# Optimization experiments

Hardware: AMD Instinct MI355X
Metric: run time of the kernel (lower is better)

## Reference

```python
import jax, jax.numpy as jnp
import numpy as np

NUM_USERS = 100000
NUM_ITEMS = 50000
EMB_DIM = 128
NUM_LAYERS = 3
NUM_EDGES = 2000000
BATCH = 8192
REG = 1e-4


def setup_inputs() -> dict:
    key = jax.random.key(0)
    ks = jax.random.split(key, 8)
    N = NUM_USERS + NUM_ITEMS
    user_emb = jax.random.normal(ks[0], (NUM_USERS, EMB_DIM), dtype=jnp.float32) * 0.01
    item_emb = jax.random.normal(ks[1], (NUM_ITEMS, EMB_DIM), dtype=jnp.float32) * 0.01
    edge_row = jax.random.randint(ks[2], (NUM_EDGES,), 0, N, dtype=jnp.int32)
    edge_col = jax.random.randint(ks[3], (NUM_EDGES,), 0, N, dtype=jnp.int32)
    # symmetric-normalized adjacency values are small positives
    edge_val = jax.random.uniform(ks[4], (NUM_EDGES,), dtype=jnp.float32) * 0.1
    user = jax.random.randint(ks[5], (BATCH,), 0, NUM_USERS, dtype=jnp.int32)
    pos = jax.random.randint(ks[6], (BATCH,), 0, NUM_ITEMS, dtype=jnp.int32)
    neg = jax.random.randint(ks[7], (BATCH,), 0, NUM_ITEMS, dtype=jnp.int32)
    return {"user_emb": user_emb, "item_emb": item_emb,
            "edge_row": edge_row, "edge_col": edge_col, "edge_val": edge_val,
            "user": user, "pos": pos, "neg": neg}


def _lightgcn_embedding(user_emb, item_emb, edge_row, edge_col, edge_val):
    N = user_emb.shape[0] + item_emb.shape[0]
    emb = jnp.concatenate([user_emb, item_emb], axis=0)  # [N, D]
    acc = emb
    for _ in range(NUM_LAYERS):
        # SpMM: out[r] += val * emb[c] for each edge (r, c)
        msg = emb[edge_col] * edge_val[:, None]  # [E, D]
        emb = jax.ops.segment_sum(msg, edge_row, num_segments=N)
        acc = acc + emb
    light = acc / jnp.float32(NUM_LAYERS + 1)  # mean over layer outputs
    return light[:NUM_USERS], light[NUM_USERS:]


def reference(user_emb, item_emb, edge_row, edge_col, edge_val, user, pos, neg):
    u_all, i_all = _lightgcn_embedding(user_emb, item_emb, edge_row, edge_col, edge_val)
    u_lat = u_all[user]          # [B, D]
    pos_lat = i_all[pos]
    neg_lat = i_all[neg]
    pos_score = jnp.sum(u_lat * pos_lat, axis=1)
    neg_score = jnp.sum(u_lat * neg_lat, axis=1)
    # L1 regularization on ego (layer-0) embeddings, scalar broadcast onto batch loss
    reg_loss = REG * (jnp.sum(jnp.abs(user_emb[user]))
                      + jnp.sum(jnp.abs(item_emb[pos]))
                      + jnp.sum(jnp.abs(item_emb[neg])))
    batch_loss = jax.nn.softplus(neg_score - pos_score) + reg_loss
    return batch_loss
```

## Files before the change

### kernel.cpp

```cpp
#include <hip/hip_runtime.h>
#include <hip/hip_bf16.h>

#define EMB_D 128
#define BSH 9
#define MAXBUCK 512
#define CHUNKP 2048

typedef float f32x2 __attribute__((ext_vector_type(2)));

__device__ __forceinline__ float bf16_raw_to_f(unsigned short h) {
    return __uint_as_float(((unsigned int)h) << 16);
}
__device__ __forceinline__ float sane(float v) {
    return (v == v && fabsf(v) < 256.0f) ? v : 0.0f;
}
__device__ __forceinline__ float load_f(const void* p, int isf32, size_t idx) {
    return isf32 ? ((const float*)p)[idx]
                 : bf16_raw_to_f(((const unsigned short*)p)[idx]);
}

__device__ __forceinline__ f32x2 cvt2_fp8(unsigned int w) {
    f32x2 r;
    asm("v_cvt_pk_f32_fp8 %0, %1" : "=v"(r) : "v"(w));
    return r;
}
__device__ __forceinline__ unsigned int enc2_fp8(float a, float b) {
    unsigned int r;
    asm("v_cvt_pk_fp8_f32 %0, %1, %2" : "=v"(r) : "v"(a), "v"(b));
    return r & 0xFFFFu;
}
__device__ __forceinline__ unsigned int fp8x4_enc(float a, float b, float c, float d) {
    return enc2_fp8(a, b) | (enc2_fp8(c, d) << 16);
}
__device__ __forceinline__ float fp8_dec_byte(unsigned int b) {
    return cvt2_fp8(b & 0xFFu).x;
}

__global__ void k_detect(const unsigned short* __restrict__ ue,
                         const unsigned short* __restrict__ ie,
                         const unsigned short* __restrict__ ev,
                         int* __restrict__ flags) {
    int a = blockIdx.x;
    const unsigned short* p = (a == 0) ? ue : (a == 1) ? ie : ev;
    int lane = threadIdx.x;
    int cnt = 0;
    #pragma unroll
    for (int k = 0; k < 16; ++k) {
        float v = bf16_raw_to_f(p[k * 64 + lane]);
        if (!(fabsf(v) < 1.0f)) cnt++;
    }
    #pragma unroll
    for (int off = 32; off > 0; off >>= 1)
        cnt += __shfl_down(cnt, off, 64);
    if (lane == 0) flags[a] = (cnt > 64) ? 1 : 0;
}

__global__ __launch_bounds__(256) void k_build_emb8(
        const void* __restrict__ ue, const void* __restrict__ ie,
        const int* __restrict__ flags,
        unsigned char* __restrict__ T, float* __restrict__ S,
        int NU, int N) {
    int gid = blockIdx.x * blockDim.x + threadIdx.x;
    int row = gid >> 5;
    if (row >= N) return;
    int l = gid & 31;
    const void* src; long r; int f;
    if (row < NU) { src = ue; r = row;      f = flags[0]; }
    else          { src = ie; r = row - NU; f = flags[1]; }
    float v0, v1, v2, v3;
    if (f) {
        float4 t = ((const float4*)src)[r * 32 + l];
        v0 = sane(t.x); v1 = sane(t.y); v2 = sane(t.z); v3 = sane(t.w);
    } else {
        ushort4 t = ((const ushort4*)src)[r * 32 + l];
        v0 = sane(bf16_raw_to_f(t.x)); v1 = sane(bf16_raw_to_f(t.y));
        v2 = sane(bf16_raw_to_f(t.z)); v3 = sane(bf16_raw_to_f(t.w));
    }
    float m = fmaxf(fmaxf(fabsf(v0), fabsf(v1)), fmaxf(fabsf(v2), fabsf(v3)));
    #pragma unroll
    for (int off = 1; off < 32; off <<= 1)
        m = fmaxf(m, __shfl_xor(m, off, 64));
    float enc = (m > 0.0f) ? 448.0f / m : 0.0f;
    ((unsigned int*)T)[(size_t)row * 32 + l] =
        fp8x4_enc(v0 * enc, v1 * enc, v2 * enc, v3 * enc);
    if (l == 0) S[row] = (m > 0.0f) ? m * (1.0f / 448.0f) : 0.0f;
}

__global__ void k_zero_flags(int* __restrict__ f, int words, float* __restrict__ reg) {
    int i = blockIdx.x * blockDim.x + threadIdx.x;
    if (i < words) f[i] = 0;
    if (i == 0) reg[0] = 0.0f;
}

__global__ void k_mark_batch(const int* __restrict__ user, const int* __restrict__ pos,
                             const int* __restrict__ neg,
                             const void* __restrict__ ue, const void* __restrict__ ie,
                             const int* __restrict__ flags, int NU, int NI,
                             unsigned char* __restrict__ flag3,
                             unsigned char* __restrict__ flag2,
                             float* __restrict__ regp) {
    __shared__ float sred[2];
    int b = blockIdx.x;
    int d = threadIdx.x;
    int ui = min(max(user[b], 0), NU - 1);
    int pi = min(max(pos[b],  0), NI - 1);
    int ni = min(max(neg[b],  0), NI - 1);
    if (d == 0) {
        flag3[ui] = 1; flag3[NU + pi] = 1; flag3[NU + ni] = 1;
        flag2[ui] = 1; flag2[NU + pi] = 1; flag2[NU + ni] = 1;
    }
    int f0 = flags[0], f1 = flags[1];
    float u = sane(load_f(ue, f0, (size_t)ui * EMB_D + d));
    float p = sane(load_f(ie, f1, (size_t)pi * EMB_D + d));
    float n = sane(load_f(ie, f1, (size_t)ni * EMB_D + d));
    float s = fabsf(u) + fabsf(p) + fabsf(n);
    #pragma unroll
    for (int off = 32; off > 0; off >>= 1)
        s += __shfl_down(s, off, 64);
    if ((d & 63) == 0) sred[d >> 6] = s;
    __syncthreads();
    if (d == 0) regp[b] = sred[0] + sred[1];
}

__global__ void k_reduce_reg(const float* __restrict__ regp, float* __restrict__ reg, int B) {
    __shared__ float ss[256];
    int t = threadIdx.x;
    float s = 0.0f;
    for (int i = t; i < B; i += 256) s += regp[i];
    ss[t] = s;
    __syncthreads();
    for (int off = 128; off > 0; off >>= 1) {
        if (t < off) ss[t] += ss[t + off];
        __syncthreads();
    }
    if (t == 0) reg[0] = ss[0];
}


__global__ __launch_bounds__(256) void k_part_count(
        const int* __restrict__ erow, const int* __restrict__ ecol,
        const unsigned char* __restrict__ flag3, unsigned char* __restrict__ flag2,
        int* __restrict__ bcnt, int E, int N, int nbuck, int NB) {
    __shared__ int lh[MAXBUCK];
    int b = blockIdx.x, t = threadIdx.x;
    for (int i = t; i < MAXBUCK; i += 256) lh[i] = 0;
    __syncthreads();
    int beg = b * CHUNKP;
    int cnt = min(CHUNKP, E - beg);
    for (int p = t; p < cnt; p += 256) {
        int e = beg + p;
        int r = min(max(erow[e], 0), N - 1);
        atomicAdd(&lh[r >> BSH], 1);
        if (flag3[r]) {
            int c = min(max(ecol[e], 0), N - 1);
            flag2[c] = 1;
        }
    }
    __syncthreads();
    for (int i = t; i < nbuck; i += 256) bcnt[(long)i * NB + b] = lh[i];
}

__global__ void k_gscan1(const int* __restrict__ a, int* __restrict__ bsums, int L) {
    __shared__ int ss[256];
    int t = threadIdx.x;
    int base = blockIdx.x * 1024 + t * 4;
    int s = 0;
    #pragma unroll
    for (int j = 0; j < 4; ++j) {
        int idx = base + j;
        if (idx < L) s += a[idx];
    }
    ss[t] = s;
    __syncthreads();
    for (int off = 128; off > 0; off >>= 1) {
        if (t < off) ss[t] += ss[t + off];
        __syncthreads();
    }
    if (t == 0) bsums[blockIdx.x] = ss[0];
}

__global__ void k_gscan2(const int* __restrict__ bsums, int* __restrict__ boffs,
                         int nb, int* __restrict__ rowptrN) {
    __shared__ int ss[256];
    int t = threadIdx.x;
    int base = t * 4;
    int c[4];
    int s = 0;
    #pragma unroll
    for (int j = 0; j < 4; ++j) {
        c[j] = (base + j < nb) ? bsums[base + j] : 0;
        s += c[j];
    }
    ss[t] = s;
    __syncthreads();
    for (int off = 1; off < 256; off <<= 1) {
        int v = (t >= off) ? ss[t - off] : 0;
        __syncthreads();
        ss[t] += v;
        __syncthreads();
    }
    int run = ss[t] - s;
    #pragma unroll
    for (int j = 0; j < 4; ++j) {
        if (base + j < nb) boffs[base + j] = run;
        run += c[j];
    }
    if (t == 255) *rowptrN = ss[255];
}

__global__ void k_gscan3(int* __restrict__ a, const int* __restrict__ boffs, int L) {
    __shared__ int ss[256];
    int t = threadIdx.x;
    int base = blockIdx.x * 1024 + t * 4;
    int c[4];
    int s = 0;
    #pragma unroll
    for (int j = 0; j < 4; ++j) {
        int idx = base + j;
        c[j] = (idx < L) ? a[idx] : 0;
        s += c[j];
    }
    ss[t] = s;
    __syncthreads();
    for (int off = 1; off < 256; off <<= 1) {
        int v = (t >= off) ? ss[t - off] : 0;
        __syncthreads();
        ss[t] += v;
        __syncthreads();
    }
    int run = boffs[blockIdx.x] + ss[t] - s;
    #pragma unroll
    for (int j = 0; j < 4; ++j) {
        int idx = base + j;
        if (idx < L) a[idx] = run;
        run += c[j];
    }
}

__global__ __launch_bounds__(256) void k_part_scatter(
        const int* __restrict__ erow, const int* __restrict__ ecol,
        const void* __restrict__ eval, const int* __restrict__ flags,
        const int* __restrict__ boff,
        unsigned int* __restrict__ part_cv, unsigned short* __restrict__ part_r,
        int E, int N, int nbuck, int NB) {
    __shared__ uint2 lrec[CHUNKP];
    __shared__ unsigned short lidx[CHUNKP];
    __shared__ int hist[MAXBUCK];
    __shared__ int bstart[MAXBUCK];
    __shared__ int ss[256];
    int b = blockIdx.x, t = threadIdx.x;
    int beg = b * CHUNKP;
    int cnt = min(CHUNKP, E - beg);
    for (int i = t; i < MAXBUCK; i += 256) hist[i] = 0;
    __syncthreads();
    int f2 = flags[2];
    for (int p = t; p < cnt; p += 256) {
        int e = beg + p;
        int r = min(max(erow[e], 0), N - 1);
        int c = min(max(ecol[e], 0), N - 1);
        float v = sane(load_f(eval, f2, e));
        if (v < 0.0f) v = 0.0f;
        unsigned int u = __float_as_uint(v);
        unsigned int vb = ((u + 0x10000u) >> 17) & 0x3FFFu;
        lrec[p] = make_uint2((unsigned int)r, ((unsigned int)c << 14) | vb);
        atomicAdd(&hist[r >> BSH], 1);
    }
    __syncthreads();
    int c0 = hist[2 * t], c1 = hist[2 * t + 1];
    int s = c0 + c1;
    ss[t] = s;
    __syncthreads();
    for (int off = 1; off < 256; off <<= 1) {
        int v = (t >= off) ? ss[t - off] : 0;
        __syncthreads();
        ss[t] += v;
        __syncthreads();
    }
    int eb = ss[t] - s;
    bstart[2 * t] = eb;
    bstart[2 * t + 1] = eb + c0;
    hist[2 * t] = eb;
    hist[2 * t + 1] = eb + c0;
    __syncthreads();
    for (int p = t; p < cnt; p += 256) {
        int bin = (int)(lrec[p].x >> BSH);
        int pos = atomicAdd(&hist[bin], 1);
        lidx[pos] = (unsigned short)p;
    }
    __syncthreads();
    for (int i = t; i < nbuck; i += 256)
        hist[i] = boff[(long)i * NB + b] - bstart[i];
    __syncthreads();
    for (int p = t; p < cnt; p += 256) {
        uint2 rec = lrec[lidx[p]];
        int bin = (int)(rec.x >> BSH);
        int o = hist[bin] + p;
        part_cv[o] = rec.y;
        part_r[o] = (unsigned short)(rec.x & 511u);
    }
}

__global__ __launch_bounds__(256) void k_build_csr(
        const unsigned int* __restrict__ part_cv,
        const unsigned short* __restrict__ part_r,
        const int* __restrict__ boff,
        int* __restrict__ row_ptr, unsigned int* __restrict__ sedge,
        int E, int N, int NB, int nbuck) {
    __shared__ int rcnt[256];
    __shared__ int rcur[256];
    __shared__ int ss[256];
    __shared__ int slow;
    int blk = blockIdx.x, t = threadIdx.x;
    int bin = blk >> 1, half = blk & 1;
    int base = boff[(long)bin * NB];
    int next = (bin + 1 < nbuck) ? boff[(long)(bin + 1) * NB] : E;
    int cnt = next - base;
    int r0 = bin << BSH;
    int rlo = half << 8;
    int nrows = min(256, max(0, min(512, N - r0) - rlo));
    rcnt[t] = 0;
    if (t == 0) slow = 0;
    __syncthreads();
    int lowc = 0;
    for (int i = t; i < cnt; i += 256) {
        int pr = part_r[base + i];
        int lp = pr - rlo;
        if (lp >= 0 && lp < 256) atomicAdd(&rcnt[lp], 1);
        else if (pr < rlo) lowc++;
    }
    #pragma unroll
    for (int off = 32; off > 0; off >>= 1)
        lowc += __shfl_down(lowc, off, 64);
    if ((t & 63) == 0 && lowc) atomicAdd(&slow, lowc);
    __syncthreads();
    int c = rcnt[t];
    ss[t] = c;
    __syncthreads();
    for (int off = 1; off < 256; off <<= 1) {
        int v = (t >= off) ? ss[t - off] : 0;
        __syncthreads();
        ss[t] += v;
        __syncthreads();
    }
    int st = ss[t] - c + slow;
    rcur[t] = st;
    __syncthreads();
    if (t < nrows) row_ptr[r0 + rlo + t] = base + st;
    for (int i = t; i < cnt; i += 256) {
        int pr = part_r[base + i];
        int lp = pr - rlo;
        if (lp >= 0 && lp < 256) {
            int pos = atomicAdd(&rcur[lp], 1);
            sedge[base + pos] = part_cv[base + i];
        }
    }
}

__global__ __launch_bounds__(256, 8) void k_spmm_csr8(
        const unsigned char* __restrict__ T, const float* __restrict__ S,
        unsigned char* __restrict__ Td, float* __restrict__ Sd,
        const int* __restrict__ row_ptr, const unsigned int* __restrict__ sedge,
        int N, const unsigned char* __restrict__ skipf, int use_skip) {
    int row = blockIdx.x * (blockDim.x >> 6) + (threadIdx.x >> 6);
    if (row >= N) return;
    if (use_skip && skipf[row] == 0) return;
    int lane = threadIdx.x & 63;
    int beg = row_ptr[row], end = row_ptr[row + 1];
    const unsigned short* Tw = (const unsigned short*)T;
    float a0 = 0.0f, a1 = 0.0f;
    int e = beg;
    for (; e + 3 < end; e += 4) {
        unsigned int s0 = sedge[e],     s1 = sedge[e + 1];
        unsigned int s2 = sedge[e + 2], s3 = sedge[e + 3];
        unsigned int c0 = s0 >> 14, c1 = s1 >> 14, c2 = s2 >> 14, c3 = s3 >> 14;
        unsigned int h0 = Tw[(size_t)c0 * 64 + lane];
        unsigned int h1 = Tw[(size_t)c1 * 64 + lane];
        unsigned int h2 = Tw[(size_t)c2 * 64 + lane];
        unsigned int h3 = Tw[(size_t)c3 * 64 + lane];
        float v0 = __uint_as_float((s0 & 0x3FFFu) << 17) * S[c0];
        float v1 = __uint_as_float((s1 & 0x3FFFu) << 17) * S[c1];
        float v2 = __uint_as_float((s2 & 0x3FFFu) << 17) * S[c2];
        float v3 = __uint_as_float((s3 & 0x3FFFu) << 17) * S[c3];
        f32x2 d;
        d = cvt2_fp8(h0); a0 += v0 * d.x; a1 += v0 * d.y;
        d = cvt2_fp8(h1); a0 += v1 * d.x; a1 += v1 * d.y;
        d = cvt2_fp8(h2); a0 += v2 * d.x; a1 += v2 * d.y;
        d = cvt2_fp8(h3); a0 += v3 * d.x; a1 += v3 * d.y;
    }
    for (; e < end; ++e) {
        unsigned int s0 = sedge[e];
        unsigned int c0 = s0 >> 14;
        unsigned int h0 = Tw[(size_t)c0 * 64 + lane];
        float v0 = __uint_as_float((s0 & 0x3FFFu) << 17) * S[c0];
        f32x2 d = cvt2_fp8(h0);
        a0 += v0 * d.x; a1 += v0 * d.y;
    }
    float m = fmaxf(fabsf(a0), fabsf(a1));
    #pragma unroll
    for (int off = 1; off < 64; off <<= 1)
        m = fmaxf(m, __shfl_xor(m, off, 64));
    float enc = (m > 0.0f) ? 448.0f / m : 0.0f;
    unsigned int w = enc2_fp8(a0 * enc, a1 * enc);
    ((unsigned short*)(Td + (size_t)row * EMB_D))[lane] = (unsigned short)w;
    if (lane == 0) Sd[row] = (m > 0.0f) ? m * (1.0f / 448.0f) : 0.0f;
}

__global__ void k_gather_final(
        const void* __restrict__ ue, const void* __restrict__ ie,
        const int* __restrict__ flags,
        const int* __restrict__ user, const int* __restrict__ pos,
        const int* __restrict__ neg, int NU, int NI,
        const unsigned char* __restrict__ T1, const float* __restrict__ S1,
        const unsigned char* __restrict__ T2, const float* __restrict__ S2,
        const unsigned char* __restrict__ T3, const float* __restrict__ S3,
        const float* __restrict__ reg, float* __restrict__ out) {
    __shared__ float sps[2], sns[2];
    int b = blockIdx.x;
    int d = threadIdx.x;
    int ui = min(max(user[b], 0), NU - 1);
    int pi = min(max(pos[b],  0), NI - 1);
    int ni = min(max(neg[b],  0), NI - 1);
    size_t ru = (size_t)ui;
    size_t rp = (size_t)NU + pi;
    size_t rn = (size_t)NU + ni;
    int f0 = flags[0], f1 = flags[1];
    float u = sane(load_f(ue, f0, ru * EMB_D + d))
            + fp8_dec_byte(T1[ru * EMB_D + d]) * S1[ru]
            + fp8_dec_byte(T2[ru * EMB_D + d]) * S2[ru]
            + fp8_dec_byte(T3[ru * EMB_D + d]) * S3[ru];
    float p = sane(load_f(ie, f1, (size_t)pi * EMB_D + d))
            + fp8_dec_byte(T1[rp * EMB_D + d]) * S1[rp]
            + fp8_dec_byte(T2[rp * EMB_D + d]) * S2[rp]
            + fp8_dec_byte(T3[rp * EMB_D + d]) * S3[rp];
    float n = sane(load_f(ie, f1, (size_t)ni * EMB_D + d))
            + fp8_dec_byte(T1[rn * EMB_D + d]) * S1[rn]
            + fp8_dec_byte(T2[rn * EMB_D + d]) * S2[rn]
            + fp8_dec_byte(T3[rn * EMB_D + d]) * S3[rn];
    float ps = u * p, ns = u * n;
    #pragma unroll
    for (int off = 32; off > 0; off >>= 1) {
        ps += __shfl_down(ps, off, 64);
        ns += __shfl_down(ns, off, 64);
    }
    if ((d & 63) == 0) { sps[d >> 6] = ps; sns[d >> 6] = ns; }
    __syncthreads();
    if (d == 0) {
        float x = ((sns[0] + sns[1]) - (sps[0] + sps[1])) * 0.0625f;
        float sp = fmaxf(x, 0.0f) + log1pf(expf(-fabsf(x)));
        out[b] = sp + 1e-4f * reg[0];
    }
}

extern "C" void kernel_launch(void* const* d_in, const int* in_sizes, int n_in,
                              void* d_out, int out_size, void* d_ws, size_t ws_size,
                              hipStream_t stream) {
    const void* ue   = d_in[0];
    const void* ie   = d_in[1];
    const int*  erow = (const int*)d_in[2];
    const int*  ecol = (const int*)d_in[3];
    const void* ev   = d_in[4];
    const int*  user = (const int*)d_in[5];
    const int*  pos  = (const int*)d_in[6];
    const int*  neg  = (const int*)d_in[7];

    int NU = in_sizes[0] / EMB_D;
    int NI = in_sizes[1] / EMB_D;
    int N  = NU + NI;
    int E  = in_sizes[2];
    int B  = in_sizes[5];

    int nbuck = (N + ((1 << BSH) - 1)) >> BSH;
    int NBp   = (E + CHUNKP - 1) / CHUNKP;
    int L     = nbuck * NBp;
    int nbL   = (L + 1023) / 1024;

    size_t T8   = (size_t)N * EMB_D;
    size_t SC   = (((size_t)N * sizeof(float)) + 15) & ~15ull;
    size_t NI4  = ((size_t)(N + 1) * sizeof(int) + 15) & ~15ull;
    size_t L4   = ((size_t)L * sizeof(int) + 15) & ~15ull;
    size_t E2   = (((size_t)E * 2) + 15) & ~15ull;
    size_t Npad = ((size_t)N + 15) & ~15ull;
    char* w = (char*)d_ws;
    int*   flags   = (int*)w;
    float* reg     = (float*)(w + 64);
    char*  q       = w + 256;
    float* regp    = (float*)q;             q += (size_t)B * sizeof(float);
    int*   row_ptr = (int*)q;               q += NI4;
    unsigned int*   part_cv = (unsigned int*)q;   q += (size_t)E * 4;
    unsigned short* part_r  = (unsigned short*)q; q += E2;
    int*   bcnt    = (int*)q;               q += L4;
    int*   bsums   = (int*)q;               q += 4096;
    int*   boffs   = (int*)q;               q += 4096;
    unsigned char* flag3 = (unsigned char*)q; q += Npad;
    unsigned char* flag2 = (unsigned char*)q; q += Npad;
    unsigned int* sedge = (unsigned int*)q; q += (size_t)E * 4;
    unsigned char* Ta = (unsigned char*)q;  q += T8;
    float*         Sa = (float*)q;          q += SC;
    unsigned char* T1 = (unsigned char*)q;  q += T8;
    float*         S1 = (float*)q;          q += SC;
    unsigned char* T2 = (unsigned char*)q;  q += T8;
    float*         S2 = (float*)q;          q += SC;
    unsigned char* T3 = (unsigned char*)q;  q += T8;
    float*         S3 = (float*)q;

    const int thr = 256;
    float* out = (float*)d_out;

    k_detect<<<3, 64, 0, stream>>>((const unsigned short*)ue, (const unsigned short*)ie,
                                   (const unsigned short*)ev, flags);
    int fwords = (int)((2 * Npad) / 4);
    k_zero_flags<<<(fwords + thr - 1) / thr, thr, 0, stream>>>((int*)flag3, fwords, reg);
    k_mark_batch<<<B, EMB_D, 0, stream>>>(user, pos, neg, ue, ie, flags, NU, NI,
                                          flag3, flag2, regp);
    k_reduce_reg<<<1, 256, 0, stream>>>(regp, reg, B);
    k_build_emb8<<<(N * 32 + thr - 1) / thr, thr, 0, stream>>>(ue, ie, flags, Ta, Sa, NU, N);

    k_part_count<<<NBp, 256, 0, stream>>>(erow, ecol, flag3, flag2, bcnt, E, N, nbuck, NBp);
    k_gscan1<<<nbL, 256, 0, stream>>>(bcnt, bsums, L);
    k_gscan2<<<1, 256, 0, stream>>>(bsums, boffs, nbL, row_ptr + N);
    k_gscan3<<<nbL, 256, 0, stream>>>(bcnt, boffs, L);
    k_part_scatter<<<NBp, 256, 0, stream>>>(erow, ecol, ev, flags, bcnt,
                                            part_cv, part_r, E, N, nbuck, NBp);
    k_build_csr<<<2 * nbuck, 256, 0, stream>>>(part_cv, part_r, bcnt, row_ptr, sedge,
                                               E, N, NBp, nbuck);

    int rows_per_block = thr / 64;
    int sgrid = (N + rows_per_block - 1) / rows_per_block;

    k_spmm_csr8<<<sgrid, thr, 0, stream>>>(Ta, Sa, T1, S1, row_ptr, sedge, N, flag2, 0);
    k_spmm_csr8<<<sgrid, thr, 0, stream>>>(T1, S1, T2, S2, row_ptr, sedge, N, flag2, 1);
    k_spmm_csr8<<<sgrid, thr, 0, stream>>>(T2, S2, T3, S3, row_ptr, sedge, N, flag3, 1);

    k_gather_final<<<B, EMB_D, 0, stream>>>(ue, ie, flags, user, pos, neg, NU, NI,
                                            T1, S1, T2, S2, T3, S3, reg, out);
}
```

Baseline: 472.0 us.

## Split each row's edges across four 16-lane groups with wide fp8 loads

The SpMM kernel now splits each wavefront into four 16-lane groups. Each group handles a strided subset of a row's edges and loads 8 fp8 values per lane as a uint2, instead of 2 bytes per lane across all 64 lanes. Partial sums are combined with cross-group shuffles before the per-row max and fp8 encode, and only group 0 writes the row. Blocks grow to 1024 threads. The intent is more independent gathers in flight per row with wider memory transactions, at the cost of extra shuffle reduction work and larger blocks.

Result: faster. 460.5 us (-2.4%).

```diff
diff --git a/kernel.cpp b/kernel.cpp
--- a/kernel.cpp
+++ b/kernel.cpp
@@ -356,7 +356,7 @@
     }
 }
 
-__global__ __launch_bounds__(256, 8) void k_spmm_csr8(
+__global__ __launch_bounds__(1024, 8) void k_spmm_csr8(
         const unsigned char* __restrict__ T, const float* __restrict__ S,
         unsigned char* __restrict__ Td, float* __restrict__ Sd,
         const int* __restrict__ row_ptr, const unsigned int* __restrict__ sedge,
@@ -365,44 +365,61 @@
     if (row >= N) return;
     if (use_skip && skipf[row] == 0) return;
     int lane = threadIdx.x & 63;
+    int ph = lane >> 4;
+    int sl = lane & 15;
     int beg = row_ptr[row], end = row_ptr[row + 1];
-    const unsigned short* Tw = (const unsigned short*)T;
-    float a0 = 0.0f, a1 = 0.0f;
-    int e = beg;
-    for (; e + 3 < end; e += 4) {
-        unsigned int s0 = sedge[e],     s1 = sedge[e + 1];
-        unsigned int s2 = sedge[e + 2], s3 = sedge[e + 3];
-        unsigned int c0 = s0 >> 14, c1 = s1 >> 14, c2 = s2 >> 14, c3 = s3 >> 14;
-        unsigned int h0 = Tw[(size_t)c0 * 64 + lane];
-        unsigned int h1 = Tw[(size_t)c1 * 64 + lane];
-        unsigned int h2 = Tw[(size_t)c2 * 64 + lane];
-        unsigned int h3 = Tw[(size_t)c3 * 64 + lane];
-        float v0 = __uint_as_float((s0 & 0x3FFFu) << 17) * S[c0];
-        float v1 = __uint_as_float((s1 & 0x3FFFu) << 17) * S[c1];
-        float v2 = __uint_as_float((s2 & 0x3FFFu) << 17) * S[c2];
-        float v3 = __uint_as_float((s3 & 0x3FFFu) << 17) * S[c3];
+    float a[8];
+    #pragma unroll
+    for (int j = 0; j < 8; ++j) a[j] = 0.0f;
+    int i = beg + ph;
+    for (; i + 4 < end; i += 8) {
+        unsigned int se0 = sedge[i];
+        unsigned int se1 = sedge[i + 4];
+        unsigned int c0 = se0 >> 14, c1 = se1 >> 14;
+        uint2 h0 = ((const uint2*)(T + (size_t)c0 * EMB_D))[sl];
+        uint2 h1 = ((const uint2*)(T + (size_t)c1 * EMB_D))[sl];
+        float vs0 = __uint_as_float((se0 & 0x3FFFu) << 17) * S[c0];
+        float vs1 = __uint_as_float((se1 & 0x3FFFu) << 17) * S[c1];
         f32x2 d;
-        d = cvt2_fp8(h0); a0 += v0 * d.x; a1 += v0 * d.y;
-        d = cvt2_fp8(h1); a0 += v1 * d.x; a1 += v1 * d.y;
-        d = cvt2_fp8(h2); a0 += v2 * d.x; a1 += v2 * d.y;
-        d = cvt2_fp8(h3); a0 += v3 * d.x; a1 += v3 * d.y;
-    }
-    for (; e < end; ++e) {
-        unsigned int s0 = sedge[e];
-        unsigned int c0 = s0 >> 14;
-        unsigned int h0 = Tw[(size_t)c0 * 64 + lane];
-        float v0 = __uint_as_float((s0 & 0x3FFFu) << 17) * S[c0];
-        f32x2 d = cvt2_fp8(h0);
-        a0 += v0 * d.x; a1 += v0 * d.y;
-    }
-    float m = fmaxf(fabsf(a0), fabsf(a1));
-    #pragma unroll
-    for (int off = 1; off < 64; off <<= 1)
-        m = fmaxf(m, __shfl_xor(m, off, 64));
-    float enc = (m > 0.0f) ? 448.0f / m : 0.0f;
-    unsigned int w = enc2_fp8(a0 * enc, a1 * enc);
-    ((unsigned short*)(Td + (size_t)row * EMB_D))[lane] = (unsigned short)w;
-    if (lane == 0) Sd[row] = (m > 0.0f) ? m * (1.0f / 448.0f) : 0.0f;
+        d = cvt2_fp8(h0.x);       a[0] += vs0 * d.x; a[1] += vs0 * d.y;
+        d = cvt2_fp8(h0.x >> 16); a[2] += vs0 * d.x; a[3] += vs0 * d.y;
+        d = cvt2_fp8(h0.y);       a[4] += vs0 * d.x; a[5] += vs0 * d.y;
+        d = cvt2_fp8(h0.y >> 16); a[6] += vs0 * d.x; a[7] += vs0 * d.y;
+        d = cvt2_fp8(h1.x);       a[0] += vs1 * d.x; a[1] += vs1 * d.y;
+        d = cvt2_fp8(h1.x >> 16); a[2] += vs1 * d.x; a[3] += vs1 * d.y;
+        d = cvt2_fp8(h1.y);       a[4] += vs1 * d.x; a[5] += vs1 * d.y;
+        d = cvt2_fp8(h1.y >> 16); a[6] += vs1 * d.x; a[7] += vs1 * d.y;
+    }
+    if (i < end) {
+        unsigned int se = sedge[i];
+        unsigned int c = se >> 14;
+        uint2 h = ((const uint2*)(T + (size_t)c * EMB_D))[sl];
+        float vs = __uint_as_float((se & 0x3FFFu) << 17) * S[c];
+        f32x2 d;
+        d = cvt2_fp8(h.x);       a[0] += vs * d.x; a[1] += vs * d.y;
+        d = cvt2_fp8(h.x >> 16); a[2] += vs * d.x; a[3] += vs * d.y;
+        d = cvt2_fp8(h.y);       a[4] += vs * d.x; a[5] += vs * d.y;
+        d = cvt2_fp8(h.y >> 16); a[6] += vs * d.x; a[7] += vs * d.y;
+    }
+    #pragma unroll
+    for (int j = 0; j < 8; ++j) {
+        a[j] += __shfl_xor(a[j], 16, 64);
+        a[j] += __shfl_xor(a[j], 32, 64);
+    }
+    float m = fmaxf(fmaxf(fmaxf(fabsf(a[0]), fabsf(a[1])), fmaxf(fabsf(a[2]), fabsf(a[3]))),
+                    fmaxf(fmaxf(fabsf(a[4]), fabsf(a[5])), fmaxf(fabsf(a[6]), fabsf(a[7]))));
+    m = fmaxf(m, __shfl_xor(m, 1, 64));
+    m = fmaxf(m, __shfl_xor(m, 2, 64));
+    m = fmaxf(m, __shfl_xor(m, 4, 64));
+    m = fmaxf(m, __shfl_xor(m, 8, 64));
+    if (ph == 0) {
+        float enc = (m > 0.0f) ? 448.0f / m : 0.0f;
+        uint2 w;
+        w.x = fp8x4_enc(a[0] * enc, a[1] * enc, a[2] * enc, a[3] * enc);
+        w.y = fp8x4_enc(a[4] * enc, a[5] * enc, a[6] * enc, a[7] * enc);
+        ((uint2*)(Td + (size_t)row * EMB_D))[sl] = w;
+        if (lane == 0) Sd[row] = (m > 0.0f) ? m * (1.0f / 448.0f) : 0.0f;
+    }
 }
 
 __global__ void k_gather_final(
@@ -524,12 +541,13 @@
     k_build_csr<<<2 * nbuck, 256, 0, stream>>>(part_cv, part_r, bcnt, row_ptr, sedge,
                                                E, N, NBp, nbuck);
 
-    int rows_per_block = thr / 64;
+    const int sthr = 1024;
+    int rows_per_block = sthr / 64;
     int sgrid = (N + rows_per_block - 1) / rows_per_block;
 
-    k_spmm_csr8<<<sgrid, thr, 0, stream>>>(Ta, Sa, T1, S1, row_ptr, sedge, N, flag2, 0);
-    k_spmm_csr8<<<sgrid, thr, 0, stream>>>(T1, S1, T2, S2, row_ptr, sedge, N, flag2, 1);
-    k_spmm_csr8<<<sgrid, thr, 0, stream>>>(T2, S2, T3, S3, row_ptr, sedge, N, flag3, 1);
+    k_spmm_csr8<<<sgrid, sthr, 0, stream>>>(Ta, Sa, T1, S1, row_ptr, sedge, N, flag2, 0);
+    k_spmm_csr8<<<sgrid, sthr, 0, stream>>>(T1, S1, T2, S2, row_ptr, sedge, N, flag2, 1);
+    k_spmm_csr8<<<sgrid, sthr, 0, stream>>>(T2, S2, T3, S3, row_ptr, sedge, N, flag3, 1);
 
     k_gather_final<<<B, EMB_D, 0, stream>>>(ue, ie, flags, user, pos, neg, NU, NI,
                                             T1, S1, T2, S2, T3, S3, reg, out);
```
